# Kernel tuning notes

Measured on AMD Instinct MI355X. Metric: run time of the kernel, lower is better.

The kernel has to match this reference:

```python
import jax, jax.numpy as jnp
import numpy as np

B, NNODE, FIN, FOUT = 64, 512, 64, 64

def setup_inputs() -> dict:
    key = jax.random.key(0)
    ks = jax.random.split(key, 8)
    stdW = 1.0 / np.sqrt(FIN)
    stdA = 1.0 / np.sqrt(FOUT)
    return {
        "X": jax.random.normal(ks[0], (B, NNODE, FIN), dtype=jnp.float32),
        "A": jax.random.uniform(ks[1], (B, NNODE, NNODE), dtype=jnp.float32),
        "N": jax.random.randint(ks[2], (B,), 1, NNODE + 1, dtype=jnp.int64),
        "W": jax.random.uniform(ks[3], (FIN, FOUT), jnp.float32, -stdW, stdW),
        "a": jax.random.uniform(ks[4], (FOUT, FOUT), jnp.float32, -stdA, stdA),
        "bias_W": jax.random.uniform(ks[5], (FOUT,), jnp.float32, -stdW, stdW),
        "bias_a": jax.random.uniform(ks[6], (NNODE,), jnp.float32, -1.0 / np.sqrt(NNODE), 1.0 / np.sqrt(NNODE)),
    }

def reference(X, A, N, W, a, bias_W, bias_a):
    # A_ = A + identity on the top-left n_atoms block (only diagonal entries)
    idx = jnp.arange(A.shape[1])
    diag_mask = (idx[None, :] < N[:, None]).astype(A.dtype)  # [B, n]
    A_ = A + jnp.einsum('bn,nm->bnm', diag_mask, jnp.eye(A.shape[1], dtype=A.dtype))
    # XW: [B, n, F_out]
    XW = jnp.einsum('bnc,cd->bnd', X, W)
    # buf[a,j,k] = sum_i a[i,j] * XW^T[a,j,k]  (einsum 'ij,ajk->ajk')
    col_sum = a.sum(axis=0)  # [F_out]
    XWT = jnp.swapaxes(XW, 1, 2)  # [B, F_out, n]
    buf = col_sum[None, :, None] * XWT
    Z = jnp.einsum('bif,bfk->bik', XW, buf) + bias_a  # [B, n, n] + [n] broadcast on last dim
    att = jnp.tanh(jnp.einsum('bij,bjk->bik', A_, Z))
    H = jnp.einsum('bij,bjd->bid', att, XW) + bias_W
    return H
```

## Files before the change

kernel.cpp:

```cpp
#include <hip/hip_runtime.h>

#define BB 64
#define NN 512
#define FD 64

typedef short bf16x8 __attribute__((ext_vector_type(8)));
typedef float f32x4 __attribute__((ext_vector_type(4)));

__device__ __forceinline__ unsigned short f2bf(float f){
    unsigned u = __builtin_bit_cast(unsigned, f);
    u += 0x7fffu + ((u >> 16) & 1u);
    return (unsigned short)(u >> 16);
}
__device__ __forceinline__ float bf2f(unsigned short h){
    unsigned u = ((unsigned)h) << 16;
    return __builtin_bit_cast(float, u);
}
__device__ __forceinline__ float fast_tanh(float x){
    float e = __expf(2.0f * x);
    return 1.0f - 2.0f * __builtin_amdgcn_rcpf(e + 1.0f);
}

__global__ __launch_bounds__(256) void k_prep(const float* __restrict__ W,
                                              const float* __restrict__ a,
                                              float* __restrict__ colsum,
                                              unsigned short* __restrict__ Wt){
    __shared__ float Wl[64][68];
    __shared__ float cpart[4][64];
    int t = threadIdx.x;
    int d = t & 63, part = t >> 6;
    float s = 0.f;
    #pragma unroll
    for (int i = 0; i < 16; i++) s += a[(part*16 + i)*64 + d];
    cpart[part][d] = s;
    int r = t >> 2, c0 = (t & 3) * 16;
    {
        const float4* src = (const float4*)&W[r*64 + c0];
        #pragma unroll
        for (int q = 0; q < 4; q++) *(float4*)&Wl[r][c0 + q*4] = src[q];
    }
    __syncthreads();
    if (part == 0) colsum[d] = cpart[0][d] + cpart[1][d] + cpart[2][d] + cpart[3][d];
    #pragma unroll
    for (int q = 0; q < 4; q++){
        ushort4 o;
        #pragma unroll
        for (int jj = 0; jj < 4; jj++)
            ((unsigned short*)&o)[jj] = f2bf(Wl[c0 + q*4 + jj][r]);
        *(ushort4*)&Wt[r*64 + c0 + q*4] = o;
    }
}

__global__ __launch_bounds__(256) void k_xw(const float* __restrict__ X,
                                            const unsigned short* __restrict__ Wt,
                                            unsigned short* __restrict__ XWh,
                                            unsigned short* __restrict__ XWt){
    __shared__ unsigned short Xl[64][72];
    __shared__ unsigned short Wtl[64][72];
    __shared__ unsigned short Cl[64][72];
    int t = threadIdx.x;
    int row0 = blockIdx.x * 64;
    int r = t >> 2, c0 = (t & 3) * 16;
    {
        const float4* src = (const float4*)&X[(row0 + r)*FD + c0];
        #pragma unroll
        for (int q = 0; q < 4; q++){
            float4 v = src[q];
            ushort4 h; h.x=f2bf(v.x); h.y=f2bf(v.y); h.z=f2bf(v.z); h.w=f2bf(v.w);
            *(ushort4*)&Xl[r][c0 + q*4] = h;
        }
        const uint4* src2 = (const uint4*)&Wt[r*64 + c0];
        *(uint4*)&Wtl[r][c0]     = src2[0];
        *(uint4*)&Wtl[r][c0 + 8] = src2[1];
    }
    __syncthreads();
    int lane = t & 63, w = t >> 6, l15 = lane & 15, quad = lane >> 4;
    f32x4 acc[4] = {{0,0,0,0},{0,0,0,0},{0,0,0,0},{0,0,0,0}};
    #pragma unroll
    for (int ks = 0; ks < 2; ks++){
        bf16x8 af = *(const bf16x8*)&Xl[w*16 + l15][ks*32 + quad*8];
        #pragma unroll
        for (int nt = 0; nt < 4; nt++){
            bf16x8 bfr = *(const bf16x8*)&Wtl[nt*16 + l15][ks*32 + quad*8];
            acc[nt] = __builtin_amdgcn_mfma_f32_16x16x32_bf16(af, bfr, acc[nt], 0, 0, 0);
        }
    }
    int b = blockIdx.x >> 3, n0 = (blockIdx.x & 7) * 64;
    #pragma unroll
    for (int nt = 0; nt < 4; nt++){
        ushort4 hv;
        #pragma unroll
        for (int rg = 0; rg < 4; rg++) ((unsigned short*)&hv)[rg] = f2bf(acc[nt][rg]);
        *(ushort4*)&XWt[(b*64 + nt*16 + l15)*NN + n0 + w*16 + quad*4] = hv;
    }
    #pragma unroll
    for (int nt = 0; nt < 4; nt++)
        #pragma unroll
        for (int rg = 0; rg < 4; rg++)
            Cl[w*16 + quad*4 + rg][nt*16 + l15] = f2bf(acc[nt][rg]);
    __syncthreads();
    {
        uint4 v0 = *(const uint4*)&Cl[r][c0];
        uint4 v1 = *(const uint4*)&Cl[r][c0 + 8];
        *(uint4*)&XWh[(row0 + r)*FD + c0]     = v0;
        *(uint4*)&XWh[(row0 + r)*FD + c0 + 8] = v1;
    }
}

__global__ __launch_bounds__(256) void k_fused(const float* __restrict__ A,
                                               const unsigned short* __restrict__ XWh,
                                               const unsigned short* __restrict__ XWt,
                                               const float* __restrict__ colsum,
                                               const int* __restrict__ Ni,
                                               const float* __restrict__ bias_a,
                                               const float* __restrict__ bias_W,
                                               float* __restrict__ H){
    __shared__ unsigned short s0[64][72];
    __shared__ unsigned short s1[64][72];
    __shared__ unsigned short Ml[64][72];
    __shared__ unsigned short Pl[64][72];
    __shared__ float rspart[64][4];
    __shared__ float rsl[64];
    __shared__ float csl[64];
    __shared__ float bl[64];
    int t = threadIdx.x;
    int b = blockIdx.y, it = blockIdx.x;
    int i0 = it * 64;
    int Nb = (Ni[1] == 0) ? Ni[2*b] : Ni[b];
    int r = t >> 2, c0 = (t & 3) * 16;
    int lane = t & 63, w = t >> 6, l15 = lane & 15, quad = lane >> 4;
    if (t < 64) csl[t] = colsum[t];
    const float* Ab = A + (b*NN + i0)*NN;

    float4 pA[4]; uint4 pB[2];
    {
        const float4* src = (const float4*)&Ab[r*NN + c0];
        #pragma unroll
        for (int q = 0; q < 4; q++) pA[q] = src[q];
        const uint4* s2 = (const uint4*)&XWt[(b*64 + r)*NN + c0];
        pB[0] = s2[0]; pB[1] = s2[1];
    }
    f32x4 acc[4] = {{0,0,0,0},{0,0,0,0},{0,0,0,0},{0,0,0,0}};
    float rs = 0.f;
    for (int c = 0; c < 8; c++){
        __syncthreads();
        #pragma unroll
        for (int q = 0; q < 4; q++){
            float4 v = pA[q];
            rs += v.x + v.y + v.z + v.w;
            ushort4 h; h.x=f2bf(v.x); h.y=f2bf(v.y); h.z=f2bf(v.z); h.w=f2bf(v.w);
            *(ushort4*)&s0[r][c0 + q*4] = h;
        }
        *(uint4*)&s1[r][c0]     = pB[0];
        *(uint4*)&s1[r][c0 + 8] = pB[1];
        __syncthreads();
        if (c < 7){
            const float4* src = (const float4*)&Ab[r*NN + (c+1)*64 + c0];
            #pragma unroll
            for (int q = 0; q < 4; q++) pA[q] = src[q];
            const uint4* s2 = (const uint4*)&XWt[(b*64 + r)*NN + (c+1)*64 + c0];
            pB[0] = s2[0]; pB[1] = s2[1];
        }
        #pragma unroll
        for (int ks = 0; ks < 2; ks++){
            bf16x8 af = *(const bf16x8*)&s0[w*16 + l15][ks*32 + quad*8];
            #pragma unroll
            for (int nt = 0; nt < 4; nt++){
                bf16x8 bfr = *(const bf16x8*)&s1[nt*16 + l15][ks*32 + quad*8];
                acc[nt] = __builtin_amdgcn_mfma_f32_16x16x32_bf16(af, bfr, acc[nt], 0, 0, 0);
            }
        }
        if (c == it){
            #pragma unroll
            for (int nt = 0; nt < 4; nt++)
                #pragma unroll
                for (int rg = 0; rg < 4; rg++){
                    int iloc = w*16 + quad*4 + rg;
                    if (i0 + iloc < Nb)
                        acc[nt][rg] += bf2f(s1[nt*16 + l15][iloc]);
                }
        }
    }
    rspart[r][t & 3] = rs;
    #pragma unroll
    for (int nt = 0; nt < 4; nt++){
        float cs = csl[nt*16 + l15];
        #pragma unroll
        for (int rg = 0; rg < 4; rg++)
            Ml[w*16 + quad*4 + rg][nt*16 + l15] = f2bf(acc[nt][rg] * cs);
    }
    __syncthreads();
    if (t < 64){
        float s = rspart[t][0] + rspart[t][1] + rspart[t][2] + rspart[t][3];
        if (i0 + t < Nb) s += 1.f;
        rsl[t] = s;
    }
    __syncthreads();
    bf16x8 maf[2];
    maf[0] = *(const bf16x8*)&Ml[w*16 + l15][quad*8];
    maf[1] = *(const bf16x8*)&Ml[w*16 + l15][32 + quad*8];
    float rs_r[4];
    #pragma unroll
    for (int rg = 0; rg < 4; rg++) rs_r[rg] = rsl[w*16 + quad*4 + rg];

    uint4 q1[2], q2[2];
    {
        const uint4* a1 = (const uint4*)&XWh[(b*NN + r)*FD + c0];
        q1[0] = a1[0]; q1[1] = a1[1];
        const uint4* a2 = (const uint4*)&XWt[(b*64 + r)*NN + c0];
        q2[0] = a2[0]; q2[1] = a2[1];
    }
    f32x4 hacc[4] = {{0,0,0,0},{0,0,0,0},{0,0,0,0},{0,0,0,0}};
    for (int jt = 0; jt < 8; jt++){
        __syncthreads();
        *(uint4*)&s0[r][c0]     = q1[0];
        *(uint4*)&s0[r][c0 + 8] = q1[1];
        *(uint4*)&s1[r][c0]     = q2[0];
        *(uint4*)&s1[r][c0 + 8] = q2[1];
        if (t < 64) bl[t] = bias_a[jt*64 + t];
        __syncthreads();
        if (jt < 7){
            const uint4* a1 = (const uint4*)&XWh[(b*NN + (jt+1)*64 + r)*FD + c0];
            q1[0] = a1[0]; q1[1] = a1[1];
            const uint4* a2 = (const uint4*)&XWt[(b*64 + r)*NN + (jt+1)*64 + c0];
            q2[0] = a2[0]; q2[1] = a2[1];
        }
        #pragma unroll
        for (int nt = 0; nt < 4; nt++){
            float bv = bl[nt*16 + l15];
            f32x4 arg = { rs_r[0]*bv, rs_r[1]*bv, rs_r[2]*bv, rs_r[3]*bv };
            #pragma unroll
            for (int ks = 0; ks < 2; ks++){
                bf16x8 bfr = *(const bf16x8*)&s0[nt*16 + l15][ks*32 + quad*8];
                arg = __builtin_amdgcn_mfma_f32_16x16x32_bf16(maf[ks], bfr, arg, 0, 0, 0);
            }
            #pragma unroll
            for (int rg = 0; rg < 4; rg++)
                Pl[w*16 + quad*4 + rg][nt*16 + l15] = f2bf(fast_tanh(arg[rg]));
        }
        __syncthreads();
        #pragma unroll
        for (int ks = 0; ks < 2; ks++){
            bf16x8 paf = *(const bf16x8*)&Pl[w*16 + l15][ks*32 + quad*8];
            #pragma unroll
            for (int dt = 0; dt < 4; dt++){
                bf16x8 bfr = *(const bf16x8*)&s1[dt*16 + l15][ks*32 + quad*8];
                hacc[dt] = __builtin_amdgcn_mfma_f32_16x16x32_bf16(paf, bfr, hacc[dt], 0, 0, 0);
            }
        }
    }
    #pragma unroll
    for (int dt = 0; dt < 4; dt++){
        float bw = bias_W[dt*16 + l15];
        #pragma unroll
        for (int rg = 0; rg < 4; rg++)
            H[(b*NN + i0 + w*16 + quad*4 + rg)*FD + dt*16 + l15] = hacc[dt][rg] + bw;
    }
}

extern "C" void kernel_launch(void* const* d_in, const int* in_sizes, int n_in,
                              void* d_out, int out_size, void* d_ws, size_t ws_size,
                              hipStream_t stream){
    const float* X      = (const float*)d_in[0];
    const float* A      = (const float*)d_in[1];
    const int*   N      = (const int*)  d_in[2];
    const float* W      = (const float*)d_in[3];
    const float* a      = (const float*)d_in[4];
    const float* bias_W = (const float*)d_in[5];
    const float* bias_a = (const float*)d_in[6];
    float* H = (float*)d_out;
    char* ws = (char*)d_ws;

    unsigned short* XWh    = (unsigned short*)(ws);
    unsigned short* XWt    = (unsigned short*)(ws + (4u<<20));
    unsigned short* Wt     = (unsigned short*)(ws + (8u<<20));
    float*          colsum = (float*)(ws + (8u<<20) + 8192);

    k_prep <<<1, 256, 0, stream>>>(W, a, colsum, Wt);
    k_xw   <<<BB * NN / 64, 256, 0, stream>>>(X, Wt, XWh, XWt);
    k_fused<<<dim3(8, BB), 256, 0, stream>>>(A, XWh, XWt, colsum, N, bias_a, bias_W, H);
}
```

Baseline: 151.7 us.

## Use 8 waves per block in fused kernel and coalesce transposed XW stores

The fused attention kernel now launches 512 threads per block. Each wave owns a 16-row by 32-column slice instead of 16x64, and the M and P scratch tiles share one LDS buffer. This doubles the waves per block, so memory and MFMA latency on the A streaming loop can overlap more. The XW projection kernel also stages its transposed output through a second LDS tile, so XWt is written with wide coalesced rows instead of scattered 8-byte stores. In exchange it uses more LDS in k_xw and pays extra synchronisation overhead per tile in the larger blocks.

```diff
diff --git a/kernel.cpp b/kernel.cpp
--- a/kernel.cpp
+++ b/kernel.cpp
@@ -58,6 +58,7 @@
     __shared__ unsigned short Xl[64][72];
     __shared__ unsigned short Wtl[64][72];
     __shared__ unsigned short Cl[64][72];
+    __shared__ unsigned short ClT[64][72];
     int t = threadIdx.x;
     int row0 = blockIdx.x * 64;
     int r = t >> 2, c0 = (t & 3) * 16;
@@ -85,29 +86,31 @@
             acc[nt] = __builtin_amdgcn_mfma_f32_16x16x32_bf16(af, bfr, acc[nt], 0, 0, 0);
         }
     }
+    #pragma unroll
+    for (int nt = 0; nt < 4; nt++)
+        #pragma unroll
+        for (int rg = 0; rg < 4; rg++){
+            unsigned short hb = f2bf(acc[nt][rg]);
+            Cl [w*16 + quad*4 + rg][nt*16 + l15] = hb;
+            ClT[nt*16 + l15][w*16 + quad*4 + rg] = hb;
+        }
+    __syncthreads();
     int b = blockIdx.x >> 3, n0 = (blockIdx.x & 7) * 64;
-    #pragma unroll
-    for (int nt = 0; nt < 4; nt++){
-        ushort4 hv;
-        #pragma unroll
-        for (int rg = 0; rg < 4; rg++) ((unsigned short*)&hv)[rg] = f2bf(acc[nt][rg]);
-        *(ushort4*)&XWt[(b*64 + nt*16 + l15)*NN + n0 + w*16 + quad*4] = hv;
-    }
-    #pragma unroll
-    for (int nt = 0; nt < 4; nt++)
-        #pragma unroll
-        for (int rg = 0; rg < 4; rg++)
-            Cl[w*16 + quad*4 + rg][nt*16 + l15] = f2bf(acc[nt][rg]);
-    __syncthreads();
     {
         uint4 v0 = *(const uint4*)&Cl[r][c0];
         uint4 v1 = *(const uint4*)&Cl[r][c0 + 8];
         *(uint4*)&XWh[(row0 + r)*FD + c0]     = v0;
         *(uint4*)&XWh[(row0 + r)*FD + c0 + 8] = v1;
     }
-}
-
-__global__ __launch_bounds__(256) void k_fused(const float* __restrict__ A,
+    {
+        uint4 v0 = *(const uint4*)&ClT[r][c0];
+        uint4 v1 = *(const uint4*)&ClT[r][c0 + 8];
+        *(uint4*)&XWt[(b*64 + r)*NN + n0 + c0]     = v0;
+        *(uint4*)&XWt[(b*64 + r)*NN + n0 + c0 + 8] = v1;
+    }
+}
+
+__global__ __launch_bounds__(512) void k_fused(const float* __restrict__ A,
                                                const unsigned short* __restrict__ XWh,
                                                const unsigned short* __restrict__ XWt,
                                                const float* __restrict__ colsum,
@@ -117,9 +120,8 @@
                                                float* __restrict__ H){
     __shared__ unsigned short s0[64][72];
     __shared__ unsigned short s1[64][72];
-    __shared__ unsigned short Ml[64][72];
-    __shared__ unsigned short Pl[64][72];
-    __shared__ float rspart[64][4];
+    __shared__ unsigned short MPl[64][72];
+    __shared__ float rspart[64][8];
     __shared__ float rsl[64];
     __shared__ float csl[64];
     __shared__ float bl[64];
@@ -127,134 +129,125 @@
     int b = blockIdx.y, it = blockIdx.x;
     int i0 = it * 64;
     int Nb = (Ni[1] == 0) ? Ni[2*b] : Ni[b];
-    int r = t >> 2, c0 = (t & 3) * 16;
+    int r8 = t >> 3, c4 = (t & 7) * 4, c8 = (t & 7) * 8;
     int lane = t & 63, w = t >> 6, l15 = lane & 15, quad = lane >> 4;
+    int wr = w & 3, wc = w >> 2;
     if (t < 64) csl[t] = colsum[t];
     const float* Ab = A + (b*NN + i0)*NN;
 
-    float4 pA[4]; uint4 pB[2];
-    {
-        const float4* src = (const float4*)&Ab[r*NN + c0];
-        #pragma unroll
-        for (int q = 0; q < 4; q++) pA[q] = src[q];
-        const uint4* s2 = (const uint4*)&XWt[(b*64 + r)*NN + c0];
-        pB[0] = s2[0]; pB[1] = s2[1];
-    }
-    f32x4 acc[4] = {{0,0,0,0},{0,0,0,0},{0,0,0,0},{0,0,0,0}};
+    float4 pA0, pA1; uint4 pB;
+    pA0 = *(const float4*)&Ab[r8*NN + c4];
+    pA1 = *(const float4*)&Ab[r8*NN + 32 + c4];
+    pB  = *(const uint4*)&XWt[(b*64 + r8)*NN + c8];
+    f32x4 acc[2] = {{0,0,0,0},{0,0,0,0}};
     float rs = 0.f;
     for (int c = 0; c < 8; c++){
         __syncthreads();
-        #pragma unroll
-        for (int q = 0; q < 4; q++){
-            float4 v = pA[q];
+        {
+            float4 v = pA0;
             rs += v.x + v.y + v.z + v.w;
             ushort4 h; h.x=f2bf(v.x); h.y=f2bf(v.y); h.z=f2bf(v.z); h.w=f2bf(v.w);
-            *(ushort4*)&s0[r][c0 + q*4] = h;
-        }
-        *(uint4*)&s1[r][c0]     = pB[0];
-        *(uint4*)&s1[r][c0 + 8] = pB[1];
+            *(ushort4*)&s0[r8][c4] = h;
+            v = pA1;
+            rs += v.x + v.y + v.z + v.w;
+            ushort4 h2; h2.x=f2bf(v.x); h2.y=f2bf(v.y); h2.z=f2bf(v.z); h2.w=f2bf(v.w);
+            *(ushort4*)&s0[r8][32 + c4] = h2;
+        }
+        *(uint4*)&s1[r8][c8] = pB;
         __syncthreads();
         if (c < 7){
-            const float4* src = (const float4*)&Ab[r*NN + (c+1)*64 + c0];
-            #pragma unroll
-            for (int q = 0; q < 4; q++) pA[q] = src[q];
-            const uint4* s2 = (const uint4*)&XWt[(b*64 + r)*NN + (c+1)*64 + c0];
-            pB[0] = s2[0]; pB[1] = s2[1];
+            pA0 = *(const float4*)&Ab[r8*NN + (c+1)*64 + c4];
+            pA1 = *(const float4*)&Ab[r8*NN + (c+1)*64 + 32 + c4];
+            pB  = *(const uint4*)&XWt[(b*64 + r8)*NN + (c+1)*64 + c8];
         }
         #pragma unroll
         for (int ks = 0; ks < 2; ks++){
-            bf16x8 af = *(const bf16x8*)&s0[w*16 + l15][ks*32 + quad*8];
-            #pragma unroll
-            for (int nt = 0; nt < 4; nt++){
-                bf16x8 bfr = *(const bf16x8*)&s1[nt*16 + l15][ks*32 + quad*8];
+            bf16x8 af = *(const bf16x8*)&s0[wr*16 + l15][ks*32 + quad*8];
+            #pragma unroll
+            for (int nt = 0; nt < 2; nt++){
+                bf16x8 bfr = *(const bf16x8*)&s1[wc*32 + nt*16 + l15][ks*32 + quad*8];
                 acc[nt] = __builtin_amdgcn_mfma_f32_16x16x32_bf16(af, bfr, acc[nt], 0, 0, 0);
             }
         }
         if (c == it){
             #pragma unroll
-            for (int nt = 0; nt < 4; nt++)
+            for (int nt = 0; nt < 2; nt++)
                 #pragma unroll
                 for (int rg = 0; rg < 4; rg++){
-                    int iloc = w*16 + quad*4 + rg;
+                    int iloc = wr*16 + quad*4 + rg;
                     if (i0 + iloc < Nb)
-                        acc[nt][rg] += bf2f(s1[nt*16 + l15][iloc]);
+                        acc[nt][rg] += bf2f(s1[wc*32 + nt*16 + l15][iloc]);
                 }
         }
     }
-    rspart[r][t & 3] = rs;
-    #pragma unroll
-    for (int nt = 0; nt < 4; nt++){
-        float cs = csl[nt*16 + l15];
+    rspart[r8][t & 7] = rs;
+    #pragma unroll
+    for (int nt = 0; nt < 2; nt++){
+        float cs = csl[wc*32 + nt*16 + l15];
         #pragma unroll
         for (int rg = 0; rg < 4; rg++)
-            Ml[w*16 + quad*4 + rg][nt*16 + l15] = f2bf(acc[nt][rg] * cs);
+            MPl[wr*16 + quad*4 + rg][wc*32 + nt*16 + l15] = f2bf(acc[nt][rg] * cs);
     }
     __syncthreads();
     if (t < 64){
-        float s = rspart[t][0] + rspart[t][1] + rspart[t][2] + rspart[t][3];
+        float s = 0.f;
+        #pragma unroll
+        for (int p = 0; p < 8; p++) s += rspart[t][p];
         if (i0 + t < Nb) s += 1.f;
         rsl[t] = s;
     }
     __syncthreads();
     bf16x8 maf[2];
-    maf[0] = *(const bf16x8*)&Ml[w*16 + l15][quad*8];
-    maf[1] = *(const bf16x8*)&Ml[w*16 + l15][32 + quad*8];
+    maf[0] = *(const bf16x8*)&MPl[wr*16 + l15][quad*8];
+    maf[1] = *(const bf16x8*)&MPl[wr*16 + l15][32 + quad*8];
     float rs_r[4];
     #pragma unroll
-    for (int rg = 0; rg < 4; rg++) rs_r[rg] = rsl[w*16 + quad*4 + rg];
-
-    uint4 q1[2], q2[2];
-    {
-        const uint4* a1 = (const uint4*)&XWh[(b*NN + r)*FD + c0];
-        q1[0] = a1[0]; q1[1] = a1[1];
-        const uint4* a2 = (const uint4*)&XWt[(b*64 + r)*NN + c0];
-        q2[0] = a2[0]; q2[1] = a2[1];
-    }
-    f32x4 hacc[4] = {{0,0,0,0},{0,0,0,0},{0,0,0,0},{0,0,0,0}};
+    for (int rg = 0; rg < 4; rg++) rs_r[rg] = rsl[wr*16 + quad*4 + rg];
+
+    uint4 q1, q2;
+    q1 = *(const uint4*)&XWh[(b*NN + r8)*FD + c8];
+    q2 = *(const uint4*)&XWt[(b*64 + r8)*NN + c8];
+    f32x4 hacc[2] = {{0,0,0,0},{0,0,0,0}};
     for (int jt = 0; jt < 8; jt++){
         __syncthreads();
-        *(uint4*)&s0[r][c0]     = q1[0];
-        *(uint4*)&s0[r][c0 + 8] = q1[1];
-        *(uint4*)&s1[r][c0]     = q2[0];
-        *(uint4*)&s1[r][c0 + 8] = q2[1];
+        *(uint4*)&s0[r8][c8] = q1;
+        *(uint4*)&s1[r8][c8] = q2;
         if (t < 64) bl[t] = bias_a[jt*64 + t];
         __syncthreads();
         if (jt < 7){
-            const uint4* a1 = (const uint4*)&XWh[(b*NN + (jt+1)*64 + r)*FD + c0];
-            q1[0] = a1[0]; q1[1] = a1[1];
-            const uint4* a2 = (const uint4*)&XWt[(b*64 + r)*NN + (jt+1)*64 + c0];
-            q2[0] = a2[0]; q2[1] = a2[1];
-        }
-        #pragma unroll
-        for (int nt = 0; nt < 4; nt++){
-            float bv = bl[nt*16 + l15];
+            q1 = *(const uint4*)&XWh[(b*NN + (jt+1)*64 + r8)*FD + c8];
+            q2 = *(const uint4*)&XWt[(b*64 + r8)*NN + (jt+1)*64 + c8];
+        }
+        #pragma unroll
+        for (int nt = 0; nt < 2; nt++){
+            float bv = bl[wc*32 + nt*16 + l15];
             f32x4 arg = { rs_r[0]*bv, rs_r[1]*bv, rs_r[2]*bv, rs_r[3]*bv };
             #pragma unroll
             for (int ks = 0; ks < 2; ks++){
-                bf16x8 bfr = *(const bf16x8*)&s0[nt*16 + l15][ks*32 + quad*8];
+                bf16x8 bfr = *(const bf16x8*)&s0[wc*32 + nt*16 + l15][ks*32 + quad*8];
                 arg = __builtin_amdgcn_mfma_f32_16x16x32_bf16(maf[ks], bfr, arg, 0, 0, 0);
             }
             #pragma unroll
             for (int rg = 0; rg < 4; rg++)
-                Pl[w*16 + quad*4 + rg][nt*16 + l15] = f2bf(fast_tanh(arg[rg]));
+                MPl[wr*16 + quad*4 + rg][wc*32 + nt*16 + l15] = f2bf(fast_tanh(arg[rg]));
         }
         __syncthreads();
         #pragma unroll
         for (int ks = 0; ks < 2; ks++){
-            bf16x8 paf = *(const bf16x8*)&Pl[w*16 + l15][ks*32 + quad*8];
-            #pragma unroll
-            for (int dt = 0; dt < 4; dt++){
-                bf16x8 bfr = *(const bf16x8*)&s1[dt*16 + l15][ks*32 + quad*8];
+            bf16x8 paf = *(const bf16x8*)&MPl[wr*16 + l15][ks*32 + quad*8];
+            #pragma unroll
+            for (int dt = 0; dt < 2; dt++){
+                bf16x8 bfr = *(const bf16x8*)&s1[wc*32 + dt*16 + l15][ks*32 + quad*8];
                 hacc[dt] = __builtin_amdgcn_mfma_f32_16x16x32_bf16(paf, bfr, hacc[dt], 0, 0, 0);
             }
         }
     }
     #pragma unroll
-    for (int dt = 0; dt < 4; dt++){
-        float bw = bias_W[dt*16 + l15];
+    for (int dt = 0; dt < 2; dt++){
+        float bw = bias_W[wc*32 + dt*16 + l15];
         #pragma unroll
         for (int rg = 0; rg < 4; rg++)
-            H[(b*NN + i0 + w*16 + quad*4 + rg)*FD + dt*16 + l15] = hacc[dt][rg] + bw;
+            H[(b*NN + i0 + wr*16 + quad*4 + rg)*FD + wc*32 + dt*16 + l15] = hacc[dt][rg] + bw;
     }
 }
 
@@ -278,5 +271,5 @@
 
     k_prep <<<1, 256, 0, stream>>>(W, a, colsum, Wt);
     k_xw   <<<BB * NN / 64, 256, 0, stream>>>(X, Wt, XWh, XWt);
-    k_fused<<<dim3(8, BB), 256, 0, stream>>>(A, XWh, XWt, colsum, N, bias_a, bias_W, H);
-}
+    k_fused<<<dim3(8, BB), 512, 0, stream>>>(A, XWh, XWt, colsum, N, bias_a, bias_W, H);
+}
```

Result: faster. 130.6 us (-13.9%).
